# Optimization experiments

Measured on AMD Instinct MI355X. Metric: run time of the kernel, lower is better.

The kernel has to match this reference:

```python
import jax, jax.numpy as jnp
import numpy as np

B, T = 256, 64
ACT, EMB = 6, 1024
S, D = 32, 32          # stoch, discrete
SF = S * D             # flattened stochastic state (1024)
DET, HID = 600, 600


def _st_sample(logit, g):
    """Gumbel-max categorical sample with straight-through gradient.
    logit, g: [B, S, D]. Returns one-hot sample [B, S, D]."""
    idx = jnp.argmax(logit + g, axis=-1)
    onehot = jax.nn.one_hot(idx, logit.shape[-1], dtype=logit.dtype)
    probs = jax.nn.softmax(logit, axis=-1)
    return onehot + probs - jax.lax.stop_gradient(probs)


def setup_inputs() -> dict:
    key = jax.random.key(0)
    ks = jax.random.split(key, 20)
    p = lambda k, shp: (jax.random.normal(k, shp, dtype=jnp.float32) * 0.02)
    inp = {
        "action": jax.random.normal(ks[0], (B, T, ACT), dtype=jnp.float32),
        "embed": jax.random.normal(ks[1], (B, T, EMB), dtype=jnp.float32),
        "noise_img": jax.random.gumbel(ks[2], (B, T, S, D), dtype=jnp.float32),
        "noise_obs": jax.random.gumbel(ks[3], (B, T, S, D), dtype=jnp.float32),
        # img1: Dense(hidden, elu) on concat([stoch, action])
        "W_img1": p(ks[4], (SF + ACT, HID)), "b_img1": jnp.zeros((HID,), jnp.float32),
        # keras GRUCell (reset_after=True): gate order z, r, h; two biases
        "Wx": p(ks[5], (HID, 3 * DET)), "Wh": p(ks[6], (DET, 3 * DET)),
        "b_in": jnp.zeros((3 * DET,), jnp.float32), "b_rec": jnp.zeros((3 * DET,), jnp.float32),
        # img2: Dense(hidden, elu); img5: Dense(stoch*discrete)
        "W_img2": p(ks[7], (DET, HID)), "b_img2": jnp.zeros((HID,), jnp.float32),
        "W_img5": p(ks[8], (HID, SF)), "b_img5": jnp.zeros((SF,), jnp.float32),
        # obs1: Dense(hidden, elu) on concat([deter, embed]); obs3: Dense(stoch*discrete)
        "W_obs1": p(ks[9], (DET + EMB, HID)), "b_obs1": jnp.zeros((HID,), jnp.float32),
        "W_obs3": p(ks[10], (HID, SF)), "b_obs3": jnp.zeros((SF,), jnp.float32),
    }
    return inp


def reference(action, embed, noise_img, noise_obs,
              W_img1, b_img1, Wx, Wh, b_in, b_rec,
              W_img2, b_img2, W_img5, b_img5,
              W_obs1, b_obs1, W_obs3, b_obs3):
    # initial state: zeros (RSSM.initial)
    stoch0 = jnp.zeros((B, SF), jnp.float32)
    deter0 = jnp.zeros((B, DET), jnp.float32)

    def step(carry, inp):
        stoch, deter = carry                       # [B,SF], [B,DET]
        a, e, g_img, g_obs = inp
        # ---- img_step (prior) ----
        x = jax.nn.elu(jnp.concatenate([stoch, a], -1) @ W_img1 + b_img1)  # [B,HID]
        gx = x @ Wx + b_in                         # [B,3*DET]
        gh = deter @ Wh + b_rec
        xz, xr, xh = jnp.split(gx, 3, -1)
        hz, hr, hh = jnp.split(gh, 3, -1)
        z = jax.nn.sigmoid(xz + hz)
        r = jax.nn.sigmoid(xr + hr)
        cand = jnp.tanh(xh + r * hh)
        deter_n = z * deter + (1.0 - z) * cand     # [B,DET]
        y = jax.nn.elu(deter_n @ W_img2 + b_img2)
        logit_prior = (y @ W_img5 + b_img5).reshape(B, S, D)
        stoch_prior = _st_sample(logit_prior, g_img).reshape(B, SF)
        # ---- obs_step (post) ----
        o = jax.nn.elu(jnp.concatenate([deter_n, e], -1) @ W_obs1 + b_obs1)
        logit_post = (o @ W_obs3 + b_obs3).reshape(B, S, D)
        stoch_post = _st_sample(logit_post, g_obs).reshape(B, SF)
        out = (logit_post.reshape(B, SF), stoch_post, deter_n,
               logit_prior.reshape(B, SF), stoch_prior)
        return (stoch_post, deter_n), out

    xs = (jnp.swapaxes(action, 0, 1), jnp.swapaxes(embed, 0, 1),
          jnp.swapaxes(noise_img, 0, 1), jnp.swapaxes(noise_obs, 0, 1))
    _, outs = jax.lax.scan(step, (stoch0, deter0), xs)
    # outs: each [T,B,*] -> [B,T,*]; concat post_logit|post_stoch|deter|prior_logit|prior_stoch
    out = jnp.concatenate([jnp.swapaxes(o, 0, 1) for o in outs], axis=-1)  # [B,T,4*SF+DET]
    return out
```

## Files before the change

### kernel.cpp

```cpp
#include <hip/hip_runtime.h>
#include <math.h>

namespace {

constexpr int B = 256, T = 64, ACTN = 6, EMB = 1024;
constexpr int S = 32, DD = 32, SFN = 1024;
constexpr int DET = 600, HID = 600;
constexpr int OUTF = 4 * SFN + DET;

__device__ __forceinline__ float elu1(float x) { return x > 0.f ? x : expm1f(x); }
__device__ __forceinline__ float sigm(float x) { return 1.f / (1.f + expf(-x)); }

__global__ void kWB(const float* __restrict__ Wx, const float* __restrict__ Wh,
                    float* __restrict__ WBm) {
    int k = blockIdx.x;
    const float* src = (k < 600) ? (Wx + (size_t)k * 1800) : (Wh + (size_t)(k - 600) * 1800);
    for (int j = threadIdx.x; j < 600; j += blockDim.x) {
        size_t o = ((size_t)j * 1200 + k) * 3;
        WBm[o + 0] = src[j];
        WBm[o + 1] = src[600 + j];
        WBm[o + 2] = src[1200 + j];
    }
}

__global__ void kWC(const float* __restrict__ W2, const float* __restrict__ Wo1,
                    float* __restrict__ WCm) {
    int k = blockIdx.x;
    for (int j = threadIdx.x; j < 1200; j += blockDim.x) {
        float v = (j < 600) ? W2[(size_t)k * 600 + j] : Wo1[(size_t)k * 600 + (j - 600)];
        WCm[(size_t)j * 600 + k] = v;
    }
}

__global__ void kWD(const float* __restrict__ W5, const float* __restrict__ Wo3,
                    float* __restrict__ WDm) {
    int k = blockIdx.x;
    for (int j = threadIdx.x; j < 2048; j += blockDim.x) {
        float v = (j < 1024) ? W5[(size_t)k * 1024 + j] : Wo3[(size_t)k * 1024 + (j - 1024)];
        WDm[(size_t)j * 600 + k] = v;
    }
}

__global__ __launch_bounds__(512) void kPemb(const float* __restrict__ embed,
                                             const float* __restrict__ Wo1,
                                             const float* __restrict__ bo1,
                                             float* __restrict__ embPre) {
    int bid = blockIdx.x;
    int jg = bid % 10;
    int r = bid / 10;
    int bg = r & 3;
    int t = r >> 2;
    int tid = threadIdx.x;
    int lane = tid & 63;
    int wid = __builtin_amdgcn_readfirstlane(tid >> 6);
    int b0 = bg * 64;
    int j0 = jg * 64 + wid * 8;
    bool active = (j0 < 600);
    __shared__ float tile[64 * 129];
    float acc[8] = {0, 0, 0, 0, 0, 0, 0, 0};
    for (int kc = 0; kc < EMB; kc += 128) {
        __syncthreads();
        for (int ii = tid; ii < 64 * 128; ii += 512) {
            int i = ii >> 7, k = ii & 127;
            tile[i * 129 + k] = embed[((size_t)(b0 + i) * T + t) * EMB + kc + k];
        }
        __syncthreads();
        if (active) {
            const float* wbase = Wo1 + (size_t)(600 + kc) * 600 + j0;
#pragma unroll 4
            for (int k = 0; k < 128; ++k) {
                float v = tile[lane * 129 + k];
                float4 wa = *(const float4*)(wbase + (size_t)k * 600);
                float4 wb = *(const float4*)(wbase + (size_t)k * 600 + 4);
                acc[0] += v * wa.x; acc[1] += v * wa.y; acc[2] += v * wa.z; acc[3] += v * wa.w;
                acc[4] += v * wb.x; acc[5] += v * wb.y; acc[6] += v * wb.z; acc[7] += v * wb.w;
            }
        }
    }
    if (active) {
#pragma unroll
        for (int c = 0; c < 8; ++c)
            embPre[((size_t)t * 600 + j0 + c) * B + b0 + lane] = acc[c] + bo1[j0 + c];
    }
}

__global__ __launch_bounds__(256) void kA(const float* __restrict__ act,
                                          const float* __restrict__ W1,
                                          const float* __restrict__ b1,
                                          const int* __restrict__ idxB,
                                          float* __restrict__ xT, int t, int first) {
    int b = blockIdx.x, tid = threadIdx.x;
    __shared__ float sa[ACTN];
    __shared__ int si[S];
    if (tid < ACTN) sa[tid] = act[((size_t)b * T + t) * ACTN + tid];
    if (!first && tid < S) si[tid] = idxB[b * S + tid];
    __syncthreads();
    for (int h = tid; h < HID; h += 256) {
        float a = b1[h];
#pragma unroll
        for (int k = 0; k < ACTN; ++k) a += sa[k] * W1[(size_t)(SFN + k) * HID + h];
        if (!first) {
#pragma unroll 8
            for (int s = 0; s < S; ++s) a += W1[(size_t)(s * DD + si[s]) * HID + h];
        }
        xT[(size_t)h * B + b] = elu1(a);
    }
}

__global__ __launch_bounds__(512) void kB(const float* __restrict__ xT,
                                          const float* __restrict__ dPrev,
                                          const float* __restrict__ WBm,
                                          const float* __restrict__ b_in,
                                          const float* __restrict__ b_rec,
                                          float* __restrict__ dNext,
                                          float* __restrict__ out, int t) {
    int tid = threadIdx.x, lane = tid & 63;
    int wid = __builtin_amdgcn_readfirstlane(tid >> 6);
    int rg = blockIdx.x & 3, jg = blockIdx.x >> 2;
    int j = jg * 8 + wid;
    int b = rg * 64 + lane;
    const float* w = WBm + (size_t)j * 3600;
    float az = 0, ar = 0, ax = 0, ah = 0;
#pragma unroll 2
    for (int k = 0; k < 600; k += 4) {
        float4 wa = *(const float4*)(w + 3 * k);
        float4 wb = *(const float4*)(w + 3 * k + 4);
        float4 wc = *(const float4*)(w + 3 * k + 8);
        float x0 = xT[(size_t)(k + 0) * B + b];
        float x1 = xT[(size_t)(k + 1) * B + b];
        float x2 = xT[(size_t)(k + 2) * B + b];
        float x3 = xT[(size_t)(k + 3) * B + b];
        az += x0 * wa.x + x1 * wa.w + x2 * wb.z + x3 * wc.y;
        ar += x0 * wa.y + x1 * wb.x + x2 * wb.w + x3 * wc.z;
        ax += x0 * wa.z + x1 * wb.y + x2 * wc.x + x3 * wc.w;
    }
    const float* w2 = w + 1800;
#pragma unroll 2
    for (int k = 0; k < 600; k += 4) {
        float4 wa = *(const float4*)(w2 + 3 * k);
        float4 wb = *(const float4*)(w2 + 3 * k + 4);
        float4 wc = *(const float4*)(w2 + 3 * k + 8);
        float x0 = dPrev[(size_t)(k + 0) * B + b];
        float x1 = dPrev[(size_t)(k + 1) * B + b];
        float x2 = dPrev[(size_t)(k + 2) * B + b];
        float x3 = dPrev[(size_t)(k + 3) * B + b];
        az += x0 * wa.x + x1 * wa.w + x2 * wb.z + x3 * wc.y;
        ar += x0 * wa.y + x1 * wb.x + x2 * wb.w + x3 * wc.z;
        ah += x0 * wa.z + x1 * wb.y + x2 * wc.x + x3 * wc.w;
    }
    float dp = dPrev[(size_t)j * B + b];
    float z = sigm(az + b_in[j] + b_rec[j]);
    float rr = sigm(ar + b_in[600 + j] + b_rec[600 + j]);
    float cand = tanhf(ax + b_in[1200 + j] + rr * (ah + b_rec[1200 + j]));
    float dn = z * dp + (1.f - z) * cand;
    dNext[(size_t)j * B + b] = dn;
    out[((size_t)b * T + t) * OUTF + 2 * SFN + j] = dn;
}

__global__ __launch_bounds__(512) void kC(const float* __restrict__ dT,
                                          const float* __restrict__ WCm,
                                          const float* __restrict__ b2,
                                          const float* __restrict__ embPre,
                                          float* __restrict__ yoT, int t) {
    int tid = threadIdx.x, lane = tid & 63;
    int wid = __builtin_amdgcn_readfirstlane(tid >> 6);
    int rg = blockIdx.x & 3, jg = blockIdx.x >> 2;
    int j0 = jg * 16 + wid * 2;
    int b = rg * 64 + lane;
    const float* w0 = WCm + (size_t)j0 * 600;
    const float* w1 = w0 + 600;
    float a0 = 0, a1 = 0;
#pragma unroll 2
    for (int k = 0; k < 600; k += 4) {
        float4 p = *(const float4*)(w0 + k);
        float4 q = *(const float4*)(w1 + k);
        float v0 = dT[(size_t)(k + 0) * B + b];
        float v1 = dT[(size_t)(k + 1) * B + b];
        float v2 = dT[(size_t)(k + 2) * B + b];
        float v3 = dT[(size_t)(k + 3) * B + b];
        a0 += v0 * p.x + v1 * p.y + v2 * p.z + v3 * p.w;
        a1 += v0 * q.x + v1 * q.y + v2 * q.z + v3 * q.w;
    }
    if (j0 < 600) {
        yoT[(size_t)j0 * B + b] = elu1(a0 + b2[j0]);
        yoT[(size_t)(j0 + 1) * B + b] = elu1(a1 + b2[j0 + 1]);
    } else {
        int je = j0 - 600;
        yoT[(size_t)j0 * B + b] = elu1(a0 + embPre[((size_t)t * 600 + je) * B + b]);
        yoT[(size_t)(j0 + 1) * B + b] = elu1(a1 + embPre[((size_t)t * 600 + je + 1) * B + b]);
    }
}

__global__ __launch_bounds__(512) void kD(const float* __restrict__ yoT,
                                          const float* __restrict__ WDm,
                                          const float* __restrict__ b5,
                                          const float* __restrict__ bo3,
                                          const float* __restrict__ gImg,
                                          const float* __restrict__ gObs,
                                          float* __restrict__ out,
                                          int* __restrict__ idxB, int t) {
    int tid = threadIdx.x, lane = tid & 63;
    int wid = __builtin_amdgcn_readfirstlane(tid >> 6);
    int rg = blockIdx.x & 3, sg = blockIdx.x >> 2;
    int post = (sg >= 32) ? 1 : 0;
    int s = post ? sg - 32 : sg;
    int b = rg * 64 + lane;
    int dloc = wid * 4;
    int jglob = post * SFN + s * DD + dloc;
    const float* src = yoT + (post ? (size_t)600 * B : 0);
    const float* w0 = WDm + (size_t)jglob * 600;
    const float* w1 = w0 + 600;
    const float* w2 = w0 + 1200;
    const float* w3 = w0 + 1800;
    float a0 = 0, a1 = 0, a2 = 0, a3 = 0;
#pragma unroll 2
    for (int k = 0; k < 600; k += 4) {
        float4 p0 = *(const float4*)(w0 + k);
        float4 p1 = *(const float4*)(w1 + k);
        float4 p2 = *(const float4*)(w2 + k);
        float4 p3 = *(const float4*)(w3 + k);
        float v0 = src[(size_t)(k + 0) * B + b];
        float v1 = src[(size_t)(k + 1) * B + b];
        float v2 = src[(size_t)(k + 2) * B + b];
        float v3 = src[(size_t)(k + 3) * B + b];
        a0 += v0 * p0.x + v1 * p0.y + v2 * p0.z + v3 * p0.w;
        a1 += v0 * p1.x + v1 * p1.y + v2 * p1.z + v3 * p1.w;
        a2 += v0 * p2.x + v1 * p2.y + v2 * p2.z + v3 * p2.w;
        a3 += v0 * p3.x + v1 * p3.y + v2 * p3.z + v3 * p3.w;
    }
    const float* bias = post ? (bo3 + s * DD) : (b5 + s * DD);
    const float* g = (post ? gObs : gImg) + ((size_t)b * T + t) * SFN + s * DD;
    size_t obase = ((size_t)b * T + t) * OUTF;
    size_t lbase = obase + (post ? 0 : (2 * SFN + DET)) + s * DD;
    float vals[4];
    float accs[4] = {a0, a1, a2, a3};
#pragma unroll
    for (int c = 0; c < 4; ++c) {
        float lg = accs[c] + bias[dloc + c];
        out[lbase + dloc + c] = lg;
        vals[c] = lg + g[dloc + c];
    }
    float bm = vals[0];
    int bi = dloc;
#pragma unroll
    for (int c = 1; c < 4; ++c)
        if (vals[c] > bm) { bm = vals[c]; bi = dloc + c; }
    __shared__ float sm[8 * 64];
    __shared__ int sx[8 * 64];
    sm[wid * 64 + lane] = bm;
    sx[wid * 64 + lane] = bi;
    __syncthreads();
    float best = sm[lane];
    int bd = sx[lane];
#pragma unroll
    for (int w = 1; w < 8; ++w) {
        float v = sm[w * 64 + lane];
        if (v > best) { best = v; bd = sx[w * 64 + lane]; }
    }
    size_t sbase = obase + (post ? SFN : (3 * SFN + DET)) + s * DD;
#pragma unroll
    for (int c = 0; c < 4; ++c)
        out[sbase + dloc + c] = (dloc + c == bd) ? 1.f : 0.f;
    if (post && wid == 0) idxB[b * S + s] = bd;
}

}

extern "C" void kernel_launch(void* const* d_in, const int* in_sizes, int n_in,
                              void* d_out, int out_size, void* d_ws, size_t ws_size,
                              hipStream_t stream) {
    const float* action = (const float*)d_in[0];
    const float* embed  = (const float*)d_in[1];
    const float* gImg   = (const float*)d_in[2];
    const float* gObs   = (const float*)d_in[3];
    const float* W1     = (const float*)d_in[4];
    const float* b1     = (const float*)d_in[5];
    const float* Wx     = (const float*)d_in[6];
    const float* Wh     = (const float*)d_in[7];
    const float* b_in   = (const float*)d_in[8];
    const float* b_rec  = (const float*)d_in[9];
    const float* W2     = (const float*)d_in[10];
    const float* b2     = (const float*)d_in[11];
    const float* W5     = (const float*)d_in[12];
    const float* b5     = (const float*)d_in[13];
    const float* Wo1    = (const float*)d_in[14];
    const float* bo1    = (const float*)d_in[15];
    const float* Wo3    = (const float*)d_in[16];
    const float* bo3    = (const float*)d_in[17];
    float* out = (float*)d_out;

    float* ws = (float*)d_ws;
    float* WBm    = ws;
    float* WCm    = WBm + 2160000;
    float* WDm    = WCm + 720000;
    float* embPre = WDm + 1228800;
    float* xT     = embPre + 9830400;
    float* dA     = xT + 153600;
    float* dB     = dA + 153600;
    float* yoT    = dB + 153600;
    int*   idxB   = (int*)(yoT + 307200);

    hipMemsetAsync(dA, 0, 153600 * sizeof(float), stream);
    kWB<<<1200, 256, 0, stream>>>(Wx, Wh, WBm);
    kWC<<<600, 256, 0, stream>>>(W2, Wo1, WCm);
    kWD<<<600, 256, 0, stream>>>(W5, Wo3, WDm);
    kPemb<<<2560, 512, 0, stream>>>(embed, Wo1, bo1, embPre);

    for (int t = 0; t < T; ++t) {
        float* dP = (t & 1) ? dB : dA;
        float* dN = (t & 1) ? dA : dB;
        kA<<<256, 256, 0, stream>>>(action, W1, b1, idxB, xT, t, t == 0 ? 1 : 0);
        kB<<<300, 512, 0, stream>>>(xT, dP, WBm, b_in, b_rec, dN, out, t);
        kC<<<300, 512, 0, stream>>>(dN, WCm, b2, embPre, yoT, t);
        kD<<<256, 512, 0, stream>>>(yoT, WDm, b5, bo3, gImg, gObs, out, idxB, t);
    }
}
```

Before: 10.56 ms.

## Fuse per-timestep kernels into one persistent kernel with grid barriers

Replaces the 256 per-step kernel launches with a single persistent kernel of 320 blocks that loops over all timesteps and separates stages with atomic-counter grid barriers. The weight layouts are repacked so each wave handles pairs of output columns, the GRU stage splits its K dimension across waves with an LDS reduction, and activations are staged through LDS tiles. The aim is to remove launch overhead and improve activation reuse. In exchange it relies on all 320 blocks being co-resident, since the spin barrier deadlocks otherwise, and the LDS staging adds extra __syncthreads.

```diff
diff --git a/kernel.cpp b/kernel.cpp
--- a/kernel.cpp
+++ b/kernel.cpp
@@ -7,28 +7,45 @@
 constexpr int S = 32, DD = 32, SFN = 1024;
 constexpr int DET = 600, HID = 600;
 constexpr int OUTF = 4 * SFN + DET;
+constexpr int KC = 60;
 
 __device__ __forceinline__ float elu1(float x) { return x > 0.f ? x : expm1f(x); }
 __device__ __forceinline__ float sigm(float x) { return 1.f / (1.f + expf(-x)); }
 
-__global__ void kWB(const float* __restrict__ Wx, const float* __restrict__ Wh,
-                    float* __restrict__ WBm) {
-    int k = blockIdx.x;
-    const float* src = (k < 600) ? (Wx + (size_t)k * 1800) : (Wh + (size_t)(k - 600) * 1800);
-    for (int j = threadIdx.x; j < 600; j += blockDim.x) {
-        size_t o = ((size_t)j * 1200 + k) * 3;
-        WBm[o + 0] = src[j];
-        WBm[o + 1] = src[600 + j];
-        WBm[o + 2] = src[1200 + j];
-    }
-}
-
-__global__ void kWC(const float* __restrict__ W2, const float* __restrict__ Wo1,
-                    float* __restrict__ WCm) {
-    int k = blockIdx.x;
-    for (int j = threadIdx.x; j < 1200; j += blockDim.x) {
-        float v = (j < 600) ? W2[(size_t)k * 600 + j] : Wo1[(size_t)k * 600 + (j - 600)];
-        WCm[(size_t)j * 600 + k] = v;
+__device__ __forceinline__ void gridBar(unsigned* bar, int slot, unsigned nblk) {
+    __syncthreads();
+    if (threadIdx.x == 0) {
+        __threadfence();
+        atomicAdd(&bar[slot], 1u);
+        while (__hip_atomic_load(&bar[slot], __ATOMIC_RELAXED, __HIP_MEMORY_SCOPE_AGENT) < nblk) {
+            __builtin_amdgcn_s_sleep(2);
+        }
+        __threadfence();
+    }
+    __syncthreads();
+}
+
+__global__ void kWB2(const float* __restrict__ Wx, const float* __restrict__ Wh,
+                     float* __restrict__ WB2) {
+    int p = blockIdx.x;
+    int j0 = 2 * p, j1 = 2 * p + 1;
+    for (int k = threadIdx.x; k < 1200; k += blockDim.x) {
+        const float* src = (k < 600) ? (Wx + (size_t)k * 1800) : (Wh + (size_t)(k - 600) * 1800);
+        float* d = WB2 + ((size_t)p * 1200 + k) * 6;
+        d[0] = src[j0]; d[1] = src[600 + j0]; d[2] = src[1200 + j0];
+        d[3] = src[j1]; d[4] = src[600 + j1]; d[5] = src[1200 + j1];
+    }
+}
+
+__global__ void kWC2(const float* __restrict__ W2, const float* __restrict__ Wo1,
+                     float* __restrict__ WC2) {
+    int p = blockIdx.x;
+    int j0 = 2 * p, j1 = j0 + 1;
+    for (int k = threadIdx.x; k < 600; k += blockDim.x) {
+        float v0 = (j0 < 600) ? W2[(size_t)k * 600 + j0] : Wo1[(size_t)k * 600 + (j0 - 600)];
+        float v1 = (j1 < 600) ? W2[(size_t)k * 600 + j1] : Wo1[(size_t)k * 600 + (j1 - 600)];
+        float* d = WC2 + ((size_t)p * 600 + k) * 2;
+        d[0] = v0; d[1] = v1;
     }
 }
 
@@ -84,184 +101,223 @@
     }
 }
 
-__global__ __launch_bounds__(256) void kA(const float* __restrict__ act,
-                                          const float* __restrict__ W1,
-                                          const float* __restrict__ b1,
-                                          const int* __restrict__ idxB,
-                                          float* __restrict__ xT, int t, int first) {
-    int b = blockIdx.x, tid = threadIdx.x;
-    __shared__ float sa[ACTN];
-    __shared__ int si[S];
-    if (tid < ACTN) sa[tid] = act[((size_t)b * T + t) * ACTN + tid];
-    if (!first && tid < S) si[tid] = idxB[b * S + tid];
-    __syncthreads();
-    for (int h = tid; h < HID; h += 256) {
-        float a = b1[h];
-#pragma unroll
-        for (int k = 0; k < ACTN; ++k) a += sa[k] * W1[(size_t)(SFN + k) * HID + h];
-        if (!first) {
-#pragma unroll 8
-            for (int s = 0; s < S; ++s) a += W1[(size_t)(s * DD + si[s]) * HID + h];
-        }
-        xT[(size_t)h * B + b] = elu1(a);
-    }
-}
-
-__global__ __launch_bounds__(512) void kB(const float* __restrict__ xT,
-                                          const float* __restrict__ dPrev,
-                                          const float* __restrict__ WBm,
-                                          const float* __restrict__ b_in,
-                                          const float* __restrict__ b_rec,
-                                          float* __restrict__ dNext,
-                                          float* __restrict__ out, int t) {
-    int tid = threadIdx.x, lane = tid & 63;
-    int wid = __builtin_amdgcn_readfirstlane(tid >> 6);
-    int rg = blockIdx.x & 3, jg = blockIdx.x >> 2;
-    int j = jg * 8 + wid;
-    int b = rg * 64 + lane;
-    const float* w = WBm + (size_t)j * 3600;
-    float az = 0, ar = 0, ax = 0, ah = 0;
-#pragma unroll 2
-    for (int k = 0; k < 600; k += 4) {
-        float4 wa = *(const float4*)(w + 3 * k);
-        float4 wb = *(const float4*)(w + 3 * k + 4);
-        float4 wc = *(const float4*)(w + 3 * k + 8);
-        float x0 = xT[(size_t)(k + 0) * B + b];
-        float x1 = xT[(size_t)(k + 1) * B + b];
-        float x2 = xT[(size_t)(k + 2) * B + b];
-        float x3 = xT[(size_t)(k + 3) * B + b];
-        az += x0 * wa.x + x1 * wa.w + x2 * wb.z + x3 * wc.y;
-        ar += x0 * wa.y + x1 * wb.x + x2 * wb.w + x3 * wc.z;
-        ax += x0 * wa.z + x1 * wb.y + x2 * wc.x + x3 * wc.w;
-    }
-    const float* w2 = w + 1800;
-#pragma unroll 2
-    for (int k = 0; k < 600; k += 4) {
-        float4 wa = *(const float4*)(w2 + 3 * k);
-        float4 wb = *(const float4*)(w2 + 3 * k + 4);
-        float4 wc = *(const float4*)(w2 + 3 * k + 8);
-        float x0 = dPrev[(size_t)(k + 0) * B + b];
-        float x1 = dPrev[(size_t)(k + 1) * B + b];
-        float x2 = dPrev[(size_t)(k + 2) * B + b];
-        float x3 = dPrev[(size_t)(k + 3) * B + b];
-        az += x0 * wa.x + x1 * wa.w + x2 * wb.z + x3 * wc.y;
-        ar += x0 * wa.y + x1 * wb.x + x2 * wb.w + x3 * wc.z;
-        ah += x0 * wa.z + x1 * wb.y + x2 * wc.x + x3 * wc.w;
-    }
-    float dp = dPrev[(size_t)j * B + b];
-    float z = sigm(az + b_in[j] + b_rec[j]);
-    float rr = sigm(ar + b_in[600 + j] + b_rec[600 + j]);
-    float cand = tanhf(ax + b_in[1200 + j] + rr * (ah + b_rec[1200 + j]));
-    float dn = z * dp + (1.f - z) * cand;
-    dNext[(size_t)j * B + b] = dn;
-    out[((size_t)b * T + t) * OUTF + 2 * SFN + j] = dn;
-}
-
-__global__ __launch_bounds__(512) void kC(const float* __restrict__ dT,
-                                          const float* __restrict__ WCm,
-                                          const float* __restrict__ b2,
-                                          const float* __restrict__ embPre,
-                                          float* __restrict__ yoT, int t) {
-    int tid = threadIdx.x, lane = tid & 63;
-    int wid = __builtin_amdgcn_readfirstlane(tid >> 6);
-    int rg = blockIdx.x & 3, jg = blockIdx.x >> 2;
-    int j0 = jg * 16 + wid * 2;
-    int b = rg * 64 + lane;
-    const float* w0 = WCm + (size_t)j0 * 600;
-    const float* w1 = w0 + 600;
-    float a0 = 0, a1 = 0;
-#pragma unroll 2
-    for (int k = 0; k < 600; k += 4) {
-        float4 p = *(const float4*)(w0 + k);
-        float4 q = *(const float4*)(w1 + k);
-        float v0 = dT[(size_t)(k + 0) * B + b];
-        float v1 = dT[(size_t)(k + 1) * B + b];
-        float v2 = dT[(size_t)(k + 2) * B + b];
-        float v3 = dT[(size_t)(k + 3) * B + b];
-        a0 += v0 * p.x + v1 * p.y + v2 * p.z + v3 * p.w;
-        a1 += v0 * q.x + v1 * q.y + v2 * q.z + v3 * q.w;
-    }
-    if (j0 < 600) {
-        yoT[(size_t)j0 * B + b] = elu1(a0 + b2[j0]);
-        yoT[(size_t)(j0 + 1) * B + b] = elu1(a1 + b2[j0 + 1]);
-    } else {
-        int je = j0 - 600;
-        yoT[(size_t)j0 * B + b] = elu1(a0 + embPre[((size_t)t * 600 + je) * B + b]);
-        yoT[(size_t)(j0 + 1) * B + b] = elu1(a1 + embPre[((size_t)t * 600 + je + 1) * B + b]);
-    }
-}
-
-__global__ __launch_bounds__(512) void kD(const float* __restrict__ yoT,
-                                          const float* __restrict__ WDm,
-                                          const float* __restrict__ b5,
-                                          const float* __restrict__ bo3,
-                                          const float* __restrict__ gImg,
-                                          const float* __restrict__ gObs,
-                                          float* __restrict__ out,
-                                          int* __restrict__ idxB, int t) {
-    int tid = threadIdx.x, lane = tid & 63;
-    int wid = __builtin_amdgcn_readfirstlane(tid >> 6);
-    int rg = blockIdx.x & 3, sg = blockIdx.x >> 2;
-    int post = (sg >= 32) ? 1 : 0;
-    int s = post ? sg - 32 : sg;
-    int b = rg * 64 + lane;
-    int dloc = wid * 4;
-    int jglob = post * SFN + s * DD + dloc;
-    const float* src = yoT + (post ? (size_t)600 * B : 0);
-    const float* w0 = WDm + (size_t)jglob * 600;
-    const float* w1 = w0 + 600;
-    const float* w2 = w0 + 1200;
-    const float* w3 = w0 + 1800;
-    float a0 = 0, a1 = 0, a2 = 0, a3 = 0;
-#pragma unroll 2
-    for (int k = 0; k < 600; k += 4) {
-        float4 p0 = *(const float4*)(w0 + k);
-        float4 p1 = *(const float4*)(w1 + k);
-        float4 p2 = *(const float4*)(w2 + k);
-        float4 p3 = *(const float4*)(w3 + k);
-        float v0 = src[(size_t)(k + 0) * B + b];
-        float v1 = src[(size_t)(k + 1) * B + b];
-        float v2 = src[(size_t)(k + 2) * B + b];
-        float v3 = src[(size_t)(k + 3) * B + b];
-        a0 += v0 * p0.x + v1 * p0.y + v2 * p0.z + v3 * p0.w;
-        a1 += v0 * p1.x + v1 * p1.y + v2 * p1.z + v3 * p1.w;
-        a2 += v0 * p2.x + v1 * p2.y + v2 * p2.z + v3 * p2.w;
-        a3 += v0 * p3.x + v1 * p3.y + v2 * p3.z + v3 * p3.w;
-    }
-    const float* bias = post ? (bo3 + s * DD) : (b5 + s * DD);
-    const float* g = (post ? gObs : gImg) + ((size_t)b * T + t) * SFN + s * DD;
-    size_t obase = ((size_t)b * T + t) * OUTF;
-    size_t lbase = obase + (post ? 0 : (2 * SFN + DET)) + s * DD;
-    float vals[4];
-    float accs[4] = {a0, a1, a2, a3};
-#pragma unroll
-    for (int c = 0; c < 4; ++c) {
-        float lg = accs[c] + bias[dloc + c];
-        out[lbase + dloc + c] = lg;
-        vals[c] = lg + g[dloc + c];
-    }
-    float bm = vals[0];
-    int bi = dloc;
-#pragma unroll
-    for (int c = 1; c < 4; ++c)
-        if (vals[c] > bm) { bm = vals[c]; bi = dloc + c; }
+__global__ __launch_bounds__(512, 4) void kMain(
+    const float* act, const float* W1, const float* b1,
+    const float* WB2, const float* b_in, const float* b_rec,
+    const float* WC2, const float* b2, const float* embPre,
+    const float* WDm, const float* b5, const float* bo3,
+    const float* gImg, const float* gObs,
+    float* xT, float* dA, float* dB, float* yoT, int* idxB,
+    unsigned* bar, float* out) {
+    int bid = blockIdx.x;
+    int tid = threadIdx.x;
+    int lane = tid & 63;
+    int ws = __builtin_amdgcn_readfirstlane(tid >> 6);
+    unsigned nblk = gridDim.x;
+
+    int xcd = bid & 7, q = bid >> 3;
+    int jgl = q % 10, rgBC = q / 10;
+    int jg = xcd + 8 * jgl;
+    bool bcActive = (jg < 75);
+    int b0BC = rgBC * 64;
+    bool dActive = (bid < 256);
+    int sg = (bid & 7) + 8 * ((bid >> 3) & 7);
+    int rgD = bid >> 6;
+    int postD = (sg >= 32) ? 1 : 0;
+    int sD = postD ? sg - 32 : sg;
+    int b0D = rgD * 64;
+
+    __shared__ float tA[KC * 64];
+    __shared__ float tB2[KC * 64];
+    __shared__ float part[4][6][64];
     __shared__ float sm[8 * 64];
     __shared__ int sx[8 * 64];
-    sm[wid * 64 + lane] = bm;
-    sx[wid * 64 + lane] = bi;
-    __syncthreads();
-    float best = sm[lane];
-    int bd = sx[lane];
-#pragma unroll
-    for (int w = 1; w < 8; ++w) {
-        float v = sm[w * 64 + lane];
-        if (v > best) { best = v; bd = sx[w * 64 + lane]; }
-    }
-    size_t sbase = obase + (post ? SFN : (3 * SFN + DET)) + s * DD;
-#pragma unroll
-    for (int c = 0; c < 4; ++c)
-        out[sbase + dloc + c] = (dloc + c == bd) ? 1.f : 0.f;
-    if (post && wid == 0) idxB[b * S + s] = bd;
+    __shared__ float shA[ACTN];
+    __shared__ int shI[S];
+
+    for (int t = 0; t < T; ++t) {
+        const float* dPrev = (t & 1) ? dB : dA;
+        float* dNext = (t & 1) ? dA : dB;
+
+        if (bid < 256) {
+            int b = bid;
+            if (tid < ACTN) shA[tid] = act[((size_t)b * T + t) * ACTN + tid];
+            if (t > 0 && tid < S) shI[tid] = idxB[b * S + tid];
+            __syncthreads();
+            for (int h = tid; h < HID; h += 512) {
+                float a = b1[h];
+#pragma unroll
+                for (int k = 0; k < ACTN; ++k) a += shA[k] * W1[(size_t)(SFN + k) * HID + h];
+                if (t > 0) {
+#pragma unroll 8
+                    for (int s = 0; s < S; ++s) a += W1[(size_t)(s * DD + shI[s]) * HID + h];
+                }
+                xT[(size_t)h * B + b] = elu1(a);
+            }
+        }
+        gridBar(bar, t * 4 + 0, nblk);
+
+        if (bcActive) {
+            int jp = ws & 3;
+            int kq = ws >> 2;
+            int jpG = jg * 4 + jp;
+            const float* w = WB2 + ((size_t)jpG * 1200 + kq * 600) * 6;
+            float a00 = 0, a01 = 0, a02 = 0, a10 = 0, a11 = 0, a12 = 0;
+            for (int c = 0; c < 600; c += KC) {
+                __syncthreads();
+                for (int i = tid; i < KC * 16 * 2; i += 512) {
+                    int hf = i >= KC * 16;
+                    int i2 = hf ? i - KC * 16 : i;
+                    int kk = i2 >> 4, qq = (i2 & 15) << 2;
+                    float4 v = *(const float4*)((hf ? dPrev : xT) + (size_t)(c + kk) * B + b0BC + qq);
+                    float* d = (hf ? tB2 : tA) + kk * 64 + qq;
+                    d[0] = v.x; d[1] = v.y; d[2] = v.z; d[3] = v.w;
+                }
+                __syncthreads();
+                const float* tl = kq ? tB2 : tA;
+                const float* wc = w + (size_t)c * 6;
+#pragma unroll 4
+                for (int kk = 0; kk < KC; ++kk) {
+                    float x = tl[kk * 64 + lane];
+                    const float* wk = wc + kk * 6;
+                    float2 u0 = *(const float2*)(wk);
+                    float2 u1 = *(const float2*)(wk + 2);
+                    float2 u2 = *(const float2*)(wk + 4);
+                    a00 += x * u0.x; a01 += x * u0.y; a02 += x * u1.x;
+                    a10 += x * u1.y; a11 += x * u2.x; a12 += x * u2.y;
+                }
+            }
+            __syncthreads();
+            if (kq) {
+                part[jp][0][lane] = a00; part[jp][1][lane] = a01; part[jp][2][lane] = a02;
+                part[jp][3][lane] = a10; part[jp][4][lane] = a11; part[jp][5][lane] = a12;
+            }
+            __syncthreads();
+            if (!kq) {
+                int b = b0BC + lane;
+#pragma unroll
+                for (int e = 0; e < 2; ++e) {
+                    int jj = jg * 8 + 2 * jp + e;
+                    float az = (e ? a10 : a00) + part[jp][e * 3 + 0][lane];
+                    float ar = (e ? a11 : a01) + part[jp][e * 3 + 1][lane];
+                    float ax = (e ? a12 : a02);
+                    float ah = part[jp][e * 3 + 2][lane];
+                    float dp = dPrev[(size_t)jj * B + b];
+                    float z = sigm(az + b_in[jj] + b_rec[jj]);
+                    float rr = sigm(ar + b_in[600 + jj] + b_rec[600 + jj]);
+                    float cand = tanhf(ax + b_in[1200 + jj] + rr * (ah + b_rec[1200 + jj]));
+                    float dn = z * dp + (1.f - z) * cand;
+                    dNext[(size_t)jj * B + b] = dn;
+                    out[((size_t)b * T + t) * OUTF + 2 * SFN + jj] = dn;
+                }
+            }
+        }
+        gridBar(bar, t * 4 + 1, nblk);
+
+        if (bcActive) {
+            int j0 = jg * 16 + 2 * ws;
+            const float* wcBase = WC2 + (size_t)(jg * 8 + ws) * 600 * 2;
+            float a0 = 0, a1 = 0;
+            for (int c = 0; c < 600; c += KC) {
+                __syncthreads();
+                for (int i = tid; i < KC * 16; i += 512) {
+                    int kk = i >> 4, qq = (i & 15) << 2;
+                    float4 v = *(const float4*)(dNext + (size_t)(c + kk) * B + b0BC + qq);
+                    float* d = tA + kk * 64 + qq;
+                    d[0] = v.x; d[1] = v.y; d[2] = v.z; d[3] = v.w;
+                }
+                __syncthreads();
+                const float* wc = wcBase + (size_t)c * 2;
+#pragma unroll 4
+                for (int kk = 0; kk < KC; ++kk) {
+                    float x = tA[kk * 64 + lane];
+                    float2 u = *(const float2*)(wc + kk * 2);
+                    a0 += x * u.x; a1 += x * u.y;
+                }
+            }
+            int b = b0BC + lane;
+            if (j0 < 600) {
+                yoT[(size_t)j0 * B + b] = elu1(a0 + b2[j0]);
+                yoT[(size_t)(j0 + 1) * B + b] = elu1(a1 + b2[j0 + 1]);
+            } else {
+                int je = j0 - 600;
+                yoT[(size_t)j0 * B + b] = elu1(a0 + embPre[((size_t)t * 600 + je) * B + b]);
+                yoT[(size_t)(j0 + 1) * B + b] = elu1(a1 + embPre[((size_t)t * 600 + je + 1) * B + b]);
+            }
+        }
+        gridBar(bar, t * 4 + 2, nblk);
+
+        if (dActive) {
+            int dloc = ws * 4;
+            int jglob = postD * SFN + sD * DD + dloc;
+            const float* src = yoT + (postD ? (size_t)600 * B : 0);
+            const float* w0 = WDm + (size_t)jglob * 600;
+            const float* w1 = w0 + 600;
+            const float* w2 = w0 + 1200;
+            const float* w3 = w0 + 1800;
+            float a0 = 0, a1 = 0, a2 = 0, a3 = 0;
+            for (int c = 0; c < 600; c += KC) {
+                __syncthreads();
+                for (int i = tid; i < KC * 16; i += 512) {
+                    int kk = i >> 4, qq = (i & 15) << 2;
+                    float4 v = *(const float4*)(src + (size_t)(c + kk) * B + b0D + qq);
+                    float* d = tA + kk * 64 + qq;
+                    d[0] = v.x; d[1] = v.y; d[2] = v.z; d[3] = v.w;
+                }
+                __syncthreads();
+#pragma unroll 2
+                for (int kk = 0; kk < KC; kk += 4) {
+                    float4 p0 = *(const float4*)(w0 + c + kk);
+                    float4 p1 = *(const float4*)(w1 + c + kk);
+                    float4 p2 = *(const float4*)(w2 + c + kk);
+                    float4 p3 = *(const float4*)(w3 + c + kk);
+                    float v0 = tA[(kk + 0) * 64 + lane];
+                    float v1 = tA[(kk + 1) * 64 + lane];
+                    float v2 = tA[(kk + 2) * 64 + lane];
+                    float v3 = tA[(kk + 3) * 64 + lane];
+                    a0 += v0 * p0.x + v1 * p0.y + v2 * p0.z + v3 * p0.w;
+                    a1 += v0 * p1.x + v1 * p1.y + v2 * p1.z + v3 * p1.w;
+                    a2 += v0 * p2.x + v1 * p2.y + v2 * p2.z + v3 * p2.w;
+                    a3 += v0 * p3.x + v1 * p3.y + v2 * p3.z + v3 * p3.w;
+                }
+            }
+            int b = b0D + lane;
+            const float* bias = postD ? (bo3 + sD * DD) : (b5 + sD * DD);
+            const float* g = (postD ? gObs : gImg) + ((size_t)b * T + t) * SFN + sD * DD;
+            size_t obase = ((size_t)b * T + t) * OUTF;
+            size_t lbase = obase + (postD ? 0 : (2 * SFN + DET)) + sD * DD;
+            float vals[4];
+            float accs[4] = {a0, a1, a2, a3};
+#pragma unroll
+            for (int c = 0; c < 4; ++c) {
+                float lg = accs[c] + bias[dloc + c];
+                out[lbase + dloc + c] = lg;
+                vals[c] = lg + g[dloc + c];
+            }
+            float bm = vals[0];
+            int bi = dloc;
+#pragma unroll
+            for (int c = 1; c < 4; ++c)
+                if (vals[c] > bm) { bm = vals[c]; bi = dloc + c; }
+            __syncthreads();
+            sm[ws * 64 + lane] = bm;
+            sx[ws * 64 + lane] = bi;
+            __syncthreads();
+            float best = sm[lane];
+            int bd = sx[lane];
+#pragma unroll
+            for (int w = 1; w < 8; ++w) {
+                float v = sm[w * 64 + lane];
+                if (v > best) { best = v; bd = sx[w * 64 + lane]; }
+            }
+            size_t sbase = obase + (postD ? SFN : (3 * SFN + DET)) + sD * DD;
+#pragma unroll
+            for (int c = 0; c < 4; ++c)
+                out[sbase + dloc + c] = (dloc + c == bd) ? 1.f : 0.f;
+            if (postD && ws == 0) idxB[b * S + sD] = bd;
+        }
+        gridBar(bar, t * 4 + 3, nblk);
+    }
 }
 
 }
@@ -290,28 +346,28 @@
     float* out = (float*)d_out;
 
     float* ws = (float*)d_ws;
-    float* WBm    = ws;
-    float* WCm    = WBm + 2160000;
-    float* WDm    = WCm + 720000;
+    float* WB2    = ws;
+    float* WC2    = WB2 + 2160000;
+    float* WDm    = WC2 + 720000;
     float* embPre = WDm + 1228800;
     float* xT     = embPre + 9830400;
     float* dA     = xT + 153600;
     float* dB     = dA + 153600;
     float* yoT    = dB + 153600;
     int*   idxB   = (int*)(yoT + 307200);
+    unsigned* bar = (unsigned*)(idxB + 8192);
 
     hipMemsetAsync(dA, 0, 153600 * sizeof(float), stream);
-    kWB<<<1200, 256, 0, stream>>>(Wx, Wh, WBm);
-    kWC<<<600, 256, 0, stream>>>(W2, Wo1, WCm);
+    hipMemsetAsync(bar, 0, 256 * sizeof(unsigned), stream);
+    kWB2<<<300, 256, 0, stream>>>(Wx, Wh, WB2);
+    kWC2<<<600, 256, 0, stream>>>(W2, Wo1, WC2);
     kWD<<<600, 256, 0, stream>>>(W5, Wo3, WDm);
     kPemb<<<2560, 512, 0, stream>>>(embed, Wo1, bo1, embPre);
 
-    for (int t = 0; t < T; ++t) {
-        float* dP = (t & 1) ? dB : dA;
-        float* dN = (t & 1) ? dA : dB;
-        kA<<<256, 256, 0, stream>>>(action, W1, b1, idxB, xT, t, t == 0 ? 1 : 0);
-        kB<<<300, 512, 0, stream>>>(xT, dP, WBm, b_in, b_rec, dN, out, t);
-        kC<<<300, 512, 0, stream>>>(dN, WCm, b2, embPre, yoT, t);
-        kD<<<256, 512, 0, stream>>>(yoT, WDm, b5, bo3, gImg, gObs, out, idxB, t);
-    }
-}
+    kMain<<<320, 512, 0, stream>>>(action, W1, b1,
+                                   WB2, b_in, b_rec,
+                                   WC2, b2, embPre,
+                                   WDm, b5, bo3,
+                                   gImg, gObs,
+                                   xT, dA, dB, yoT, idxB, bar, out);
+}
```

Measured after the change: 22.84 ms. 116% more time.
